# Optimization experiments

Hardware: AMD Instinct MI355X
Metric: run time of the kernel (lower is better)

Reference implementation:

```python
import jax, jax.numpy as jnp
import numpy as np

B = 16        # graphs per protein batch
NPG = 2000    # nodes per graph
N = B * NPG   # total nodes
E = 640000    # total edges
H, C = 3, 128 # heads, hidden_dim
FIN = 1038
K = 400       # ceil(0.2 * NPG) SAGPool keep count
NEG = 0.1     # LeakyReLU slope in model
EPS = 1e-5


def setup_inputs() -> dict:
    key = jax.random.key(0)
    ks = jax.random.split(key, 24)
    d = {}
    d['p1_x'] = jax.random.normal(ks[0], (N, FIN), jnp.float32)
    d['p2_x'] = jax.random.normal(ks[1], (N, FIN), jnp.float32)
    d['p1_edge_index'] = jax.random.randint(ks[2], (2, E), 0, N, jnp.int32)
    d['p2_edge_index'] = jax.random.randint(ks[3], (2, E), 0, N, jnp.int32)
    d['p1_edge_attr'] = jax.random.uniform(ks[4], (E, 2), jnp.float32)
    d['p2_edge_attr'] = jax.random.uniform(ks[5], (E, 2), jnp.float32)
    s_in = 1.0 / np.sqrt(FIN)
    s_h = 1.0 / np.sqrt(C)
    # GATv2Conv params (lin_l has bias, lin_r no bias, lin_edge, att, out bias)
    d['Wl'] = jax.random.normal(ks[6], (FIN, H * C), jnp.float32) * s_in
    d['bl'] = jnp.zeros((H * C,), jnp.float32)
    d['Wr'] = jax.random.normal(ks[7], (FIN, H * C), jnp.float32) * s_in
    d['We'] = jax.random.normal(ks[8], (2, H * C), jnp.float32) * 0.5
    d['att'] = jax.random.normal(ks[9], (H, C), jnp.float32) * s_h
    d['conv_bias'] = jnp.zeros((C,), jnp.float32)
    # BatchNorm1d
    d['gamma'] = jnp.ones((C,), jnp.float32)
    d['beta'] = jnp.zeros((C,), jnp.float32)
    # SAGPooling scorer: GraphConv(C -> 1)
    d['gc_Wrel'] = jax.random.normal(ks[10], (C, 1), jnp.float32) * s_h
    d['gc_Wroot'] = jax.random.normal(ks[11], (C, 1), jnp.float32) * s_h
    d['gc_b'] = jnp.zeros((1,), jnp.float32)
    # MLP head
    d['W1'] = jax.random.normal(ks[12], (2 * C, C), jnp.float32) / np.sqrt(2 * C)
    d['b1'] = jnp.zeros((C,), jnp.float32)
    d['W2'] = jax.random.normal(ks[13], (C, C // 2), jnp.float32) * s_h
    d['b2'] = jnp.zeros((C // 2,), jnp.float32)
    d['Wo'] = jax.random.normal(ks[14], (C // 2, 1), jnp.float32) / np.sqrt(C // 2)
    d['bo'] = jnp.zeros((1,), jnp.float32)
    return d


def gatv2(x, ei, ea, Wl, bl, Wr, We, att, conv_bias):
    # GATv2Conv, heads=3, concat=False, edge_dim=2, add_self_loops (fill='mean')
    loop = jnp.arange(N, dtype=ei.dtype)
    src = jnp.concatenate([ei[0], loop])
    dst = jnp.concatenate([ei[1], loop])
    ea_full = jnp.concatenate([ea, jnp.broadcast_to(ea.mean(0), (N, ea.shape[1]))], 0)
    xl = (x @ Wl + bl).reshape(N, H, C)
    xr = (x @ Wr).reshape(N, H, C)
    ef = (ea_full @ We).reshape(-1, H, C)
    m = xl[src] + xr[dst] + ef                      # [E+N, H, C]
    e = jnp.einsum('ehc,hc->eh', jax.nn.leaky_relu(m, 0.2), att)
    emax = jax.ops.segment_max(e, dst, num_segments=N)
    ex = jnp.exp(e - emax[dst])
    denom = jax.ops.segment_sum(ex, dst, num_segments=N)
    alpha = ex / denom[dst]                          # softmax per dst node, per head
    out = jax.ops.segment_sum(alpha[:, :, None] * xl[src], dst, num_segments=N)
    return out.mean(1) + conv_bias                   # concat=False -> head mean


def branch(x, ei, ea, Wl, bl, Wr, We, att, conv_bias, gamma, beta,
           gc_Wrel, gc_Wroot, gc_b):
    h = gatv2(x, ei, ea, Wl, bl, Wr, We, att, conv_bias)
    h = jax.nn.leaky_relu(h, NEG)
    mu = h.mean(0)
    var = ((h - mu) ** 2).mean(0)
    h = (h - mu) / jnp.sqrt(var + EPS) * gamma + beta  # BatchNorm1d (batch stats)
    # SAGPooling scorer: GraphConv out_i = W_root x_i + W_rel sum_{j->i} x_j + b
    agg = jax.ops.segment_sum(h[ei[0]], ei[1], num_segments=N)
    score = jnp.tanh((h @ gc_Wroot + agg @ gc_Wrel + gc_b)[:, 0])  # [N]
    s = score.reshape(B, NPG)
    topv, topi = jax.lax.top_k(s, K)                 # per-graph top-k
    hb = h.reshape(B, NPG, C)
    hsel = jnp.take_along_axis(hb, topi[:, :, None], axis=1)  # [B, K, C]
    hsel = hsel * topv[:, :, None]                   # x[perm] * tanh(score)[perm]
    return hsel.mean(1)                              # global mean pool -> [B, C]


def reference(p1_x, p2_x, p1_edge_attr, p2_edge_attr, Wl, bl, Wr, We, att,
              conv_bias, gamma, beta, gc_Wrel, gc_Wroot, gc_b, W1, b1, W2, b2,
              Wo, bo, p1_edge_index, p2_edge_index):
    x1 = branch(p1_x, p1_edge_index, p1_edge_attr, Wl, bl, Wr, We, att,
                conv_bias, gamma, beta, gc_Wrel, gc_Wroot, gc_b)
    x2 = branch(p2_x, p2_edge_index, p2_edge_attr, Wl, bl, Wr, We, att,
                conv_bias, gamma, beta, gc_Wrel, gc_Wroot, gc_b)
    xc = jnp.concatenate([x1, x2], 1)                # [B, 2C]
    xc = jax.nn.leaky_relu(xc @ W1 + b1, NEG)
    xc = jax.nn.leaky_relu(xc @ W2 + b2, NEG)
    return jax.nn.sigmoid(xc @ Wo + bo)              # [B, 1]
```

## Files before the change

kernel.cpp:

```cpp
#include <hip/hip_runtime.h>
#include <hip/hip_bf16.h>
#include <math.h>

#define NN 32000
#define EE 640000
#define CC 128
#define HC 384
#define FIN 1038
#define KP 1056
#define KT 33
#define BB 16
#define NPG 2000
#define KK 400

#define XLR_H  12288000u
#define HBN_STR 4096000u
#define OFF_STR 32064u

#define XH_OFF     0u
#define XL_OFF     16896000u
#define XR_OFF     29184000u
#define HBN_OFF    41472000u
#define SED_OFF    49664000u
#define CNT_OFF    52224000u
#define BNSUM_OFF  52288000u
#define BNSQ_OFF   52288256u
#define MEANEA_OFF 52288512u
#define ZERO_BYTES ((52288516u - 52224000u) * 4u)
#define OFFS_OFF   52288576u
#define CUR_OFF    52352704u
#define R_OFF      52416704u
#define REL_OFF    52480704u
#define SCORE_OFF  52544704u
#define XB_OFF     52608704u
#define WTH_OFF    52612800u

typedef __attribute__((ext_vector_type(8))) _Float16 f16x8;
typedef __attribute__((ext_vector_type(2))) _Float16 f16x2;
typedef __attribute__((ext_vector_type(4))) float f32x4;
typedef __attribute__((ext_vector_type(8))) unsigned short us8;

typedef const __attribute__((address_space(1))) unsigned int* gp1_t;
typedef __attribute__((address_space(3))) unsigned int* lp3_t;
__device__ __forceinline__ void gl_lds16(const void* g, void* l) {
    __builtin_amdgcn_global_load_lds((gp1_t)g, (lp3_t)l, 16, 0, 0);
}

__global__ __launch_bounds__(256) void k_prep(const int* __restrict__ ei0, const int* __restrict__ ei1,
                                              const float* __restrict__ ea0, const float* __restrict__ ea1,
                                              int* __restrict__ cnt, float* __restrict__ meanea) {
    int b = blockIdx.x;
    int br = (b >= 2500);
    int tid = threadIdx.x;
    int e = (b - br * 2500) * 256 + tid;
    const int* ei = br ? ei1 : ei0;
    const float* ea = br ? ea1 : ea0;
    cnt += br * NN; meanea += br * 2;
    float s0 = 0.f, s1 = 0.f;
    if (e < EE) {
        atomicAdd(&cnt[ei[EE + e]], 1);
        float2 t = ((const float2*)ea)[e];
        s0 = t.x; s1 = t.y;
    }
    __shared__ float r0[256], r1[256];
    r0[tid] = s0; r1[tid] = s1; __syncthreads();
    for (int st = 128; st; st >>= 1) {
        if (tid < st) { r0[tid] += r0[tid + st]; r1[tid] += r1[tid + st]; }
        __syncthreads();
    }
    if (tid == 0) { atomicAdd(&meanea[0], r0[0]); atomicAdd(&meanea[1], r1[0]); }
}

__global__ __launch_bounds__(1024) void k_scan(const int* __restrict__ cnt, int* __restrict__ offs, int* __restrict__ cur) {
    int br = blockIdx.x;
    cnt += br * NN; offs += br * OFF_STR; cur += br * NN;
    __shared__ int sb[1024];
    int tid = threadIdx.x;
    int base = tid * 32;
    int s = 0;
    for (int i = 0; i < 32; i++) { int idx = base + i; s += (idx < NN) ? cnt[idx] : 0; }
    sb[tid] = s; __syncthreads();
    for (int off = 1; off < 1024; off <<= 1) {
        int v = (tid >= off) ? sb[tid - off] : 0;
        __syncthreads();
        sb[tid] += v;
        __syncthreads();
    }
    int run = sb[tid] - s;
    for (int i = 0; i < 32; i++) {
        int idx = base + i;
        if (idx < NN) { int c = cnt[idx]; offs[idx] = run; cur[idx] = run; run += c; }
    }
    if (tid == 1023) offs[NN] = run;
}

__global__ __launch_bounds__(256) void k_scatter(const int* __restrict__ ei0, const int* __restrict__ ei1,
                                                 const float* __restrict__ ea0, const float* __restrict__ ea1,
                                                 int* __restrict__ cur, int2* __restrict__ sed) {
    int b = blockIdx.x;
    int br = (b >= 2500);
    int e = (b - br * 2500) * 256 + threadIdx.x;
    const int* ei = br ? ei1 : ei0;
    const float* ea = br ? ea1 : ea0;
    cur += br * NN; sed += br * EE;
    if (e < EE) {
        int d = ei[EE + e];
        int p = atomicAdd(&cur[d], 1);
        float2 t = ((const float2*)ea)[e];
        f16x2 h; h[0] = (_Float16)t.x; h[1] = (_Float16)t.y;
        int2 pk;
        pk.x = ei[e];
        pk.y = __builtin_bit_cast(int, h);
        sed[p] = pk;
    }
}

__global__ __launch_bounds__(256) void k_cvtW(const float* __restrict__ Wl_, const float* __restrict__ Wr_,
                                              unsigned short* __restrict__ Bh) {
    int idx = blockIdx.x * 256 + threadIdx.x;
    if (idx >= 768 * (KP / 8)) return;
    int n = idx / (KP / 8);
    int seg = idx - n * (KP / 8);
    int c0 = seg * 8;
    const float* W = (n < HC) ? Wl_ : Wr_;
    int nc = (n < HC) ? n : n - HC;
    us8 h8;
#pragma unroll
    for (int j = 0; j < 8; ++j) {
        int k = c0 + j;
        float v = (k < FIN) ? W[(size_t)k * HC + nc] : 0.f;
        _Float16 h = (_Float16)v;
        h8[j] = __builtin_bit_cast(unsigned short, h);
    }
    *(us8*)&Bh[(size_t)n * KP + c0] = h8;
}

__global__ __launch_bounds__(256) void k_cvtX(const float* __restrict__ x, _Float16* __restrict__ xh) {
    int idx = blockIdx.x * 256 + threadIdx.x;
    if (idx >= NN * (KP / 8)) return;
    int row = idx / (KP / 8);
    int c8 = idx - row * (KP / 8);
    int col = c8 * 8;
    const float* gp = x + (size_t)row * FIN + col;
    f16x8 o;
    if (col + 8 <= FIN) {
        float2 v01 = ((const float2*)gp)[0];
        float2 v23 = ((const float2*)gp)[1];
        float2 v45 = ((const float2*)gp)[2];
        float2 v67 = ((const float2*)gp)[3];
        o[0] = (_Float16)v01.x; o[1] = (_Float16)v01.y;
        o[2] = (_Float16)v23.x; o[3] = (_Float16)v23.y;
        o[4] = (_Float16)v45.x; o[5] = (_Float16)v45.y;
        o[6] = (_Float16)v67.x; o[7] = (_Float16)v67.y;
    } else {
#pragma unroll
        for (int j = 0; j < 8; ++j) o[j] = (_Float16)((col + j < FIN) ? gp[j] : 0.f);
    }
    *(f16x8*)&xh[(size_t)row * KP + col] = o;
}

__global__ __launch_bounds__(256) void k_gemm3(const _Float16* __restrict__ xh,
                                               const unsigned short* __restrict__ Bh,
                                               const float* __restrict__ bias, int br,
                                               float* __restrict__ ws) {
    __shared__ _Float16 sA[128 * 32], sB[128 * 32];
    const int b2 = blockIdx.x;
    const int xcd = b2 & 7, slot = b2 >> 3;
    const int t = xcd * 188 + slot;
    if (t >= 1500) return;
    const int mt = t / 6, nt = t - mt * 6;
    const int bm = mt * 128, bn = nt * 128;

    _Float16* xlh = (_Float16*)(ws + XL_OFF) + (size_t)br * XLR_H;
    _Float16* xrh = (_Float16*)(ws + XR_OFF) + (size_t)br * XLR_H;

    const int tid = threadIdx.x;
    const int wave = tid >> 6, lane = tid & 63;
    const int wm = (wave >> 1) * 64, wn = (wave & 1) * 64;
    const int quad = lane >> 4, l15 = lane & 15;

    const int srow = wave * 16 + (lane >> 2);
    const int scol = (lane & 3) * 8;
    const size_t gA0 = (size_t)(bm + srow) * KP + scol;
    const size_t gA1 = (size_t)(bm + 64 + srow) * KP + scol;
    const size_t gB0 = (size_t)(bn + srow) * KP + scol;
    const size_t gB1 = (size_t)(bn + 64 + srow) * KP + scol;
    const int lds0 = (wave * 16) * 32 + lane * 8;
    const int lds1 = (64 + wave * 16) * 32 + lane * 8;

    f32x4 acc[4][4];
#pragma unroll
    for (int i = 0; i < 4; ++i)
#pragma unroll
        for (int j = 0; j < 4; ++j) {
            f32x4 z = {0.f, 0.f, 0.f, 0.f};
            acc[i][j] = z;
        }

    const int aoff0 = (wm + l15) * 32 + quad * 8;
    const int boff0 = (wn + l15) * 32 + quad * 8;

    for (int kt = 0; kt < KT; ++kt) {
        const int kc = kt * 32;
        gl_lds16(xh + gA0 + kc, &sA[lds0]);
        gl_lds16(xh + gA1 + kc, &sA[lds1]);
        gl_lds16(Bh + gB0 + kc, &sB[lds0]);
        gl_lds16(Bh + gB1 + kc, &sB[lds1]);
        __syncthreads();
        f16x8 bfr[4];
#pragma unroll
        for (int j = 0; j < 4; ++j) bfr[j] = *(const f16x8*)&sB[boff0 + j * 512];
#pragma unroll
        for (int i = 0; i < 4; ++i) {
            f16x8 a = *(const f16x8*)&sA[aoff0 + i * 512];
#pragma unroll
            for (int j = 0; j < 4; ++j)
                acc[i][j] = __builtin_amdgcn_mfma_f32_16x16x32_f16(a, bfr[j], acc[i][j], 0, 0, 0);
        }
        __syncthreads();
    }

    const bool isL = (nt < 3);
    if (isL) {
#pragma unroll
        for (int j = 0; j < 4; ++j) {
            const int ncol = wn + j * 16 + l15;
            const float bj = bias[bn + ncol];
#pragma unroll
            for (int i = 0; i < 4; ++i) {
#pragma unroll
                for (int r = 0; r < 4; ++r) {
                    int m = bm + wm + i * 16 + quad * 4 + r;
                    xlh[(size_t)m * HC + bn + ncol] = (_Float16)(acc[i][j][r] + bj);
                }
            }
        }
    } else {
        const int nbase = bn - HC;
#pragma unroll
        for (int j = 0; j < 4; ++j) {
            const int ncol = wn + j * 16 + l15;
#pragma unroll
            for (int i = 0; i < 4; ++i) {
#pragma unroll
                for (int r = 0; r < 4; ++r) {
                    int m = bm + wm + i * 16 + quad * 4 + r;
                    xrh[(size_t)m * HC + nbase + ncol] = (_Float16)acc[i][j][r];
                }
            }
        }
    }
}

__global__ __launch_bounds__(256) void k_gat(const unsigned short* __restrict__ xlhb, const unsigned short* __restrict__ xrhb,
                                             const int* __restrict__ offsb, const int2* __restrict__ sedb,
                                             const float* __restrict__ meaneab,
                                             const float* __restrict__ We, const float* __restrict__ att,
                                             const float* __restrict__ conv_bias, float* __restrict__ houtb) {
    int gwave = (blockIdx.x * 256 + threadIdx.x) >> 6;
    int lane = threadIdx.x & 63;
    int half = lane >> 5, l32 = lane & 31;
    int br = (gwave >= NN);
    int node = gwave - br * NN;
    const _Float16* xlh = (const _Float16*)xlhb + (size_t)br * XLR_H;
    const _Float16* xrh = (const _Float16*)xrhb + (size_t)br * XLR_H;
    const int* offs = offsb + br * OFF_STR;
    const int2* sed = sedb + br * EE;
    const float* meanea = meaneab + br * 2;
    float* hout = houtb + br * HBN_STR;

    f16x2 we0p[6], we1p[6], attp[6], xrp[6];
    const f16x2* xrw = (const f16x2*)(xrh + (size_t)node * HC);
#pragma unroll
    for (int jj = 0; jj < 6; ++jj) {
        int q = l32 + 32 * jj;
        float2 w0 = ((const float2*)We)[q];
        float2 w1 = ((const float2*)(We + HC))[q];
        float2 av = ((const float2*)att)[q];
        we0p[jj][0] = (_Float16)w0.x; we0p[jj][1] = (_Float16)w0.y;
        we1p[jj][0] = (_Float16)w1.x; we1p[jj][1] = (_Float16)w1.y;
        attp[jj][0] = (_Float16)av.x; attp[jj][1] = (_Float16)av.y;
        xrp[jj] = xrw[q];
    }
    _Float16 meh0 = (_Float16)(meanea[0] * (1.0f / EE));
    _Float16 meh1 = (_Float16)(meanea[1] * (1.0f / EE));

    int p0 = offs[node], p1 = offs[node + 1];
    int cntE = p1 - p0;
    int iters = (cntE + 2) >> 1;

    float den0 = 0.f, den1 = 0.f, den2 = 0.f;
    float accv[12];
#pragma unroll
    for (int k = 0; k < 12; ++k) accv[k] = 0.f;

    const f16x2 zero2 = {(_Float16)0.f, (_Float16)0.f};
    const f16x2 c02 = {(_Float16)0.2f, (_Float16)0.2f};

    for (int i = 0; i < iters; ++i) {
        int t = 2 * i + half;
        bool self = (t == 0);
        bool valid = (t <= cntE);
        int p = p0 + t - 1;
        if (p < p0) p = p0;
        if (p > EE - 1) p = EE - 1;
        int2 pk = sed[p];
        f16x2 eh = __builtin_bit_cast(f16x2, pk.y);
        int s = self ? node : pk.x;
        _Float16 e0 = self ? meh0 : eh[0];
        _Float16 e1 = self ? meh1 : eh[1];
        f16x2 e0p, e1p;
        e0p[0] = e0; e0p[1] = e0;
        e1p[0] = e1; e1p[1] = e1;

        const f16x2* xrow = (const f16x2*)(xlh + (size_t)s * HC);
        f16x2 xv[6];
#pragma unroll
        for (int jj = 0; jj < 6; ++jj) xv[jj] = xrow[l32 + 32 * jj];

        float pr0 = 0.f, pr1 = 0.f, pr2 = 0.f;
#pragma unroll
        for (int jj = 0; jj < 6; ++jj) {
            f16x2 u = xrp[jj] + e0p * we0p[jj];
            u = u + e1p * we1p[jj];
            f16x2 m = xv[jj] + u;
            f16x2 mx = __builtin_elementwise_max(m, zero2);
            f16x2 mn = __builtin_elementwise_min(m, zero2);
            f16x2 lk = mx + mn * c02;
#if __has_builtin(__builtin_amdgcn_fdot2)
            if (jj < 2)      pr0 = __builtin_amdgcn_fdot2(lk, attp[jj], pr0, false);
            else if (jj < 4) pr1 = __builtin_amdgcn_fdot2(lk, attp[jj], pr1, false);
            else             pr2 = __builtin_amdgcn_fdot2(lk, attp[jj], pr2, false);
#else
            float c = (float)lk[0] * (float)attp[jj][0] + (float)lk[1] * (float)attp[jj][1];
            if (jj < 2) pr0 += c; else if (jj < 4) pr1 += c; else pr2 += c;
#endif
        }
#pragma unroll
        for (int msk = 16; msk; msk >>= 1) {
            pr0 += __shfl_xor(pr0, msk);
            pr1 += __shfl_xor(pr1, msk);
            pr2 += __shfl_xor(pr2, msk);
        }
        float w0 = valid ? __expf(pr0) : 0.f;
        float w1 = valid ? __expf(pr1) : 0.f;
        float w2 = valid ? __expf(pr2) : 0.f;
        den0 += w0; den1 += w1; den2 += w2;
#pragma unroll
        for (int jj = 0; jj < 6; ++jj) {
            float wh = (jj < 2) ? w0 : ((jj < 4) ? w1 : w2);
            accv[2 * jj]     += wh * (float)xv[jj][0];
            accv[2 * jj + 1] += wh * (float)xv[jj][1];
        }
    }

#pragma unroll
    for (int k = 0; k < 12; ++k) accv[k] += __shfl_xor(accv[k], 32);
    den0 += __shfl_xor(den0, 32);
    den1 += __shfl_xor(den1, 32);
    den2 += __shfl_xor(den2, 32);

    if (half == 0) {
        float i0 = 1.f / den0, i1 = 1.f / den1, i2 = 1.f / den2;
#pragma unroll
        for (int jja = 0; jja < 2; ++jja) {
#pragma unroll
            for (int b = 0; b < 2; ++b) {
                int c = (((jja * 32 + l32) << 1) | b);
                float o = (accv[2 * jja + b] * i0 + accv[2 * (jja + 2) + b] * i1 +
                           accv[2 * (jja + 4) + b] * i2) * (1.f / 3.f) + conv_bias[c];
                o = (o > 0.f) ? o : 0.1f * o;
                hout[(size_t)node * CC + c] = o;
            }
        }
    }
}

__global__ __launch_bounds__(256) void k_bnstats(const float* __restrict__ hb, float* __restrict__ bnsumb, float* __restrict__ bnsqb) {
    int b = blockIdx.x;
    int br = b >> 9, lb = b & 511;
    const float* h = hb + br * HBN_STR;
    float* bnsum = bnsumb + br * CC;
    float* bnsq = bnsqb + br * CC;
    int c = threadIdx.x & 127;
    int row0 = lb * 2 + (threadIdx.x >> 7);
    float s = 0.f, ss = 0.f;
    for (int n = row0; n < NN; n += 1024) {
        float v = h[(size_t)n * CC + c];
        s += v; ss += v * v;
    }
    atomicAdd(&bnsum[c], s);
    atomicAdd(&bnsq[c], ss);
}

__global__ __launch_bounds__(256) void k_bnapply(float* __restrict__ hb, const float* __restrict__ bnsumb,
                                                 const float* __restrict__ bnsqb,
                                                 const float* __restrict__ gamma, const float* __restrict__ beta,
                                                 const float* __restrict__ wroot,
                                                 const float* __restrict__ wrel, float* __restrict__ r_b, float* __restrict__ rel_b) {
    int gwave = (blockIdx.x * 256 + threadIdx.x) >> 6;
    int lane = threadIdx.x & 63;
    int br = (gwave >= NN);
    int wave = gwave - br * NN;
    float* h = hb + br * HBN_STR;
    const float* bnsum = bnsumb + br * CC;
    const float* bnsq = bnsqb + br * CC;
    float* r_ = r_b + br * NN;
    float* rel_ = rel_b + br * NN;

    float mu0 = bnsum[lane] * (1.f / NN);
    float var0 = bnsq[lane] * (1.f / NN) - mu0 * mu0;
    float sc0 = gamma[lane] * rsqrtf(var0 + 1e-5f);
    float sh0 = beta[lane] - mu0 * sc0;
    float mu1 = bnsum[64 + lane] * (1.f / NN);
    float var1 = bnsq[64 + lane] * (1.f / NN) - mu1 * mu1;
    float sc1 = gamma[64 + lane] * rsqrtf(var1 + 1e-5f);
    float sh1 = beta[64 + lane] - mu1 * sc1;

    size_t base = (size_t)wave * CC;
    float v0 = h[base + lane], v1 = h[base + 64 + lane];
    v0 = v0 * sc0 + sh0;
    v1 = v1 * sc1 + sh1;
    h[base + lane] = v0;
    h[base + 64 + lane] = v1;
    float pr = v0 * wroot[lane] + v1 * wroot[64 + lane];
    float pl = v0 * wrel[lane] + v1 * wrel[64 + lane];
#pragma unroll
    for (int m = 32; m; m >>= 1) {
        pr += __shfl_xor(pr, m);
        pl += __shfl_xor(pl, m);
    }
    if (lane == 0) { r_[wave] = pr; rel_[wave] = pl; }
}

__global__ __launch_bounds__(256) void k_score(const float* __restrict__ r_b, const float* __restrict__ rel_b,
                                               const int* __restrict__ offsb, const int2* __restrict__ sedb,
                                               const float* __restrict__ gcb, float* __restrict__ scoreb) {
    int gwave = (blockIdx.x * 256 + threadIdx.x) >> 6;
    int lane = threadIdx.x & 63;
    int br = (gwave >= NN);
    int wave = gwave - br * NN;
    const float* r_ = r_b + br * NN;
    const float* rel_ = rel_b + br * NN;
    const int* offs = offsb + br * OFF_STR;
    const int2* sed = sedb + br * EE;
    float* score = scoreb + br * NN;
    int p0 = offs[wave], p1 = offs[wave + 1];
    float s = 0.f;
    for (int p = p0 + lane; p < p1; p += 64) s += rel_[sed[p].x];
#pragma unroll
    for (int m = 32; m; m >>= 1) s += __shfl_xor(s, m);
    if (lane == 0) score[wave] = tanhf(r_[wave] + s + gcb[0]);
}

__global__ __launch_bounds__(1024) void k_topk(const float* __restrict__ scoreb, const float* __restrict__ hb,
                                               float* __restrict__ xbout) {
    __shared__ float sv[2048];
    __shared__ int si[2048];
    __shared__ float red[8][128];
    int b = blockIdx.x, tid = threadIdx.x;
    int br = b >> 4, g = b & 15;
    const float* score = scoreb + br * NN;
    const float* h = hb + br * HBN_STR;
    for (int i = tid; i < 2048; i += 1024) {
        sv[i] = (i < NPG) ? score[g * NPG + i] : -2.0f;
        si[i] = i;
    }
    __syncthreads();
    for (int k = 2; k <= 2048; k <<= 1) {
        for (int j = k >> 1; j > 0; j >>= 1) {
            for (int t = tid; t < 2048; t += 1024) {
                int ixj = t ^ j;
                if (ixj > t) {
                    bool up = ((t & k) == 0);
                    float a = sv[t], bv = sv[ixj];
                    bool sw = up ? (a < bv) : (a > bv);
                    if (sw) {
                        sv[t] = bv; sv[ixj] = a;
                        int tmp = si[t]; si[t] = si[ixj]; si[ixj] = tmp;
                    }
                }
            }
            __syncthreads();
        }
    }
    int grp = tid >> 7, c = tid & 127;
    float a = 0.f;
    for (int kk = grp; kk < KK; kk += 8) {
        int node = g * NPG + si[kk];
        a += sv[kk] * h[(size_t)node * CC + c];
    }
    red[grp][c] = a;
    __syncthreads();
    if (tid < 128) {
        float v = (red[0][tid] + red[1][tid] + red[2][tid] + red[3][tid] +
                   red[4][tid] + red[5][tid] + red[6][tid] + red[7][tid]) * (1.f / KK);
        xbout[(br * BB + g) * CC + tid] = v;
    }
}

__global__ __launch_bounds__(128) void k_mlp(const float* __restrict__ xb, const float* __restrict__ W1,
                                             const float* __restrict__ b1, const float* __restrict__ W2,
                                             const float* __restrict__ b2, const float* __restrict__ Wo,
                                             const float* __restrict__ bo, float* __restrict__ out) {
    int g = blockIdx.x, tid = threadIdx.x;
    __shared__ float xc[256], l1[128], l2[64];
    xc[tid] = xb[g * CC + tid];
    xc[128 + tid] = xb[BB * CC + g * CC + tid];
    __syncthreads();
    float s = b1[tid];
    for (int i = 0; i < 256; i++) s += xc[i] * W1[i * 128 + tid];
    l1[tid] = (s > 0.f) ? s : 0.1f * s;
    __syncthreads();
    if (tid < 64) {
        float s2 = b2[tid];
        for (int i = 0; i < 128; i++) s2 += l1[i] * W2[i * 64 + tid];
        l2[tid] = (s2 > 0.f) ? s2 : 0.1f * s2;
    }
    __syncthreads();
    if (tid < 64) {
        float p = l2[tid] * Wo[tid];
#pragma unroll
        for (int m = 32; m; m >>= 1) p += __shfl_xor(p, m);
        if (tid == 0) out[g] = 1.f / (1.f + __expf(-(p + bo[0])));
    }
}

extern "C" void kernel_launch(void* const* d_in, const int* in_sizes, int n_in,
                              void* d_out, int out_size, void* d_ws, size_t ws_size,
                              hipStream_t stream) {
    (void)in_sizes; (void)n_in; (void)out_size; (void)ws_size;
    const float* x0   = (const float*)d_in[0];
    const float* x1   = (const float*)d_in[1];
    const int*   ei0  = (const int*)d_in[2];
    const int*   ei1  = (const int*)d_in[3];
    const float* ea0  = (const float*)d_in[4];
    const float* ea1  = (const float*)d_in[5];
    const float* Wl   = (const float*)d_in[6];
    const float* bl   = (const float*)d_in[7];
    const float* Wr   = (const float*)d_in[8];
    const float* We   = (const float*)d_in[9];
    const float* att  = (const float*)d_in[10];
    const float* cb   = (const float*)d_in[11];
    const float* gam  = (const float*)d_in[12];
    const float* bet  = (const float*)d_in[13];
    const float* wrel = (const float*)d_in[14];
    const float* wroot= (const float*)d_in[15];
    const float* gcb  = (const float*)d_in[16];
    const float* W1   = (const float*)d_in[17];
    const float* b1   = (const float*)d_in[18];
    const float* W2   = (const float*)d_in[19];
    const float* b2   = (const float*)d_in[20];
    const float* Wo   = (const float*)d_in[21];
    const float* bo   = (const float*)d_in[22];

    float* ws = (float*)d_ws;
    _Float16* xh  = (_Float16*)(ws + XH_OFF);
    unsigned short* xlh = (unsigned short*)(ws + XL_OFF);
    unsigned short* xrh = (unsigned short*)(ws + XR_OFF);
    float*  hbn   = ws + HBN_OFF;
    int2*   sed   = (int2*)(ws + SED_OFF);
    int*    cnt   = (int*)(ws + CNT_OFF);
    float*  bnsum = ws + BNSUM_OFF;
    float*  bnsq  = ws + BNSQ_OFF;
    float*  meanea= ws + MEANEA_OFF;
    int*    offs  = (int*)(ws + OFFS_OFF);
    int*    cur   = (int*)(ws + CUR_OFF);
    float*  r_    = ws + R_OFF;
    float*  rel_  = ws + REL_OFF;
    float*  score = ws + SCORE_OFF;
    float*  xb    = ws + XB_OFF;
    unsigned short* Wth = (unsigned short*)(ws + WTH_OFF);

    hipMemsetAsync(cnt, 0, ZERO_BYTES, stream);
    k_cvtW<<<(768 * (KP / 8) + 255) / 256, 256, 0, stream>>>(Wl, Wr, Wth);

    k_prep<<<5000, 256, 0, stream>>>(ei0, ei1, ea0, ea1, cnt, meanea);
    k_scan<<<2, 1024, 0, stream>>>(cnt, offs, cur);
    k_scatter<<<5000, 256, 0, stream>>>(ei0, ei1, ea0, ea1, cur, sed);

    k_cvtX<<<(NN * (KP / 8) + 255) / 256, 256, 0, stream>>>(x0, xh);
    k_gemm3<<<1504, 256, 0, stream>>>(xh, Wth, bl, 0, ws);
    k_cvtX<<<(NN * (KP / 8) + 255) / 256, 256, 0, stream>>>(x1, xh);
    k_gemm3<<<1504, 256, 0, stream>>>(xh, Wth, bl, 1, ws);

    k_gat<<<16000, 256, 0, stream>>>(xlh, xrh, offs, sed, meanea, We, att, cb, hbn);

    k_bnstats<<<1024, 256, 0, stream>>>(hbn, bnsum, bnsq);
    k_bnapply<<<16000, 256, 0, stream>>>(hbn, bnsum, bnsq, gam, bet, wroot, wrel, r_, rel_);
    k_score<<<16000, 256, 0, stream>>>(r_, rel_, offs, sed, gcb, score);
    k_topk<<<32, 1024, 0, stream>>>(score, hbn, xb);

    k_mlp<<<BB, 128, 0, stream>>>(xb, W1, b1, W2, b2, Wo, bo, (float*)d_out);
}
```

Before: 1.153 ms.

## Double-buffer GEMM LDS tiles, permute xl/xr layout, halve score wave width

The GEMM now double-buffers its LDS tiles and issues the next K-slice's global-to-LDS loads before computing the current one, which halves the barriers per iteration and overlaps load latency with MFMA work. The GEMM epilogue writes xl/xr columns in a permuted order so each GAT lane reads 12 contiguous halves as three 8-byte vector loads instead of six strided 4-byte loads. The score kernel uses 32 lanes per node instead of 64, halving the grid and cutting idle lanes for low-degree nodes. The costs are double the LDS footprint in the GEMM and more scattered stores in the GEMM epilogue.

```diff
diff --git a/kernel.cpp b/kernel.cpp
--- a/kernel.cpp
+++ b/kernel.cpp
@@ -36,6 +36,7 @@
 #define WTH_OFF    52612800u
 
 typedef __attribute__((ext_vector_type(8))) _Float16 f16x8;
+typedef __attribute__((ext_vector_type(4))) _Float16 f16x4;
 typedef __attribute__((ext_vector_type(2))) _Float16 f16x2;
 typedef __attribute__((ext_vector_type(4))) float f32x4;
 typedef __attribute__((ext_vector_type(8))) unsigned short us8;
@@ -44,6 +45,11 @@
 typedef __attribute__((address_space(3))) unsigned int* lp3_t;
 __device__ __forceinline__ void gl_lds16(const void* g, void* l) {
     __builtin_amdgcn_global_load_lds((gp1_t)g, (lp3_t)l, 16, 0, 0);
+}
+
+__device__ __forceinline__ int permoff(int c) {
+    int q = c >> 1, b = c & 1;
+    return ((((q & 31) * 6) + (q >> 5)) << 1) | b;
 }
 
 __global__ __launch_bounds__(256) void k_prep(const int* __restrict__ ei0, const int* __restrict__ ei1,
@@ -163,7 +169,7 @@
                                                const unsigned short* __restrict__ Bh,
                                                const float* __restrict__ bias, int br,
                                                float* __restrict__ ws) {
-    __shared__ _Float16 sA[128 * 32], sB[128 * 32];
+    __shared__ _Float16 sA[2][128 * 32], sB[2][128 * 32];
     const int b2 = blockIdx.x;
     const int xcd = b2 & 7, slot = b2 >> 3;
     const int t = xcd * 188 + slot;
@@ -200,25 +206,33 @@
     const int aoff0 = (wm + l15) * 32 + quad * 8;
     const int boff0 = (wn + l15) * 32 + quad * 8;
 
+#define STAGE(KT_, BUF_) do {                          \
+        const int kc_ = (KT_) * 32;                    \
+        gl_lds16(xh + gA0 + kc_, &sA[BUF_][lds0]);     \
+        gl_lds16(xh + gA1 + kc_, &sA[BUF_][lds1]);     \
+        gl_lds16(Bh + gB0 + kc_, &sB[BUF_][lds0]);     \
+        gl_lds16(Bh + gB1 + kc_, &sB[BUF_][lds1]);     \
+    } while (0)
+
+    STAGE(0, 0);
+    __syncthreads();
+
     for (int kt = 0; kt < KT; ++kt) {
-        const int kc = kt * 32;
-        gl_lds16(xh + gA0 + kc, &sA[lds0]);
-        gl_lds16(xh + gA1 + kc, &sA[lds1]);
-        gl_lds16(Bh + gB0 + kc, &sB[lds0]);
-        gl_lds16(Bh + gB1 + kc, &sB[lds1]);
-        __syncthreads();
+        const int cur = kt & 1, nxt = cur ^ 1;
+        if (kt + 1 < KT) STAGE(kt + 1, nxt);
         f16x8 bfr[4];
 #pragma unroll
-        for (int j = 0; j < 4; ++j) bfr[j] = *(const f16x8*)&sB[boff0 + j * 512];
+        for (int j = 0; j < 4; ++j) bfr[j] = *(const f16x8*)&sB[cur][boff0 + j * 512];
 #pragma unroll
         for (int i = 0; i < 4; ++i) {
-            f16x8 a = *(const f16x8*)&sA[aoff0 + i * 512];
+            f16x8 a = *(const f16x8*)&sA[cur][aoff0 + i * 512];
 #pragma unroll
             for (int j = 0; j < 4; ++j)
                 acc[i][j] = __builtin_amdgcn_mfma_f32_16x16x32_f16(a, bfr[j], acc[i][j], 0, 0, 0);
         }
         __syncthreads();
     }
+#undef STAGE
 
     const bool isL = (nt < 3);
     if (isL) {
@@ -226,12 +240,13 @@
         for (int j = 0; j < 4; ++j) {
             const int ncol = wn + j * 16 + l15;
             const float bj = bias[bn + ncol];
+            const int off = permoff(bn + ncol);
 #pragma unroll
             for (int i = 0; i < 4; ++i) {
 #pragma unroll
                 for (int r = 0; r < 4; ++r) {
                     int m = bm + wm + i * 16 + quad * 4 + r;
-                    xlh[(size_t)m * HC + bn + ncol] = (_Float16)(acc[i][j][r] + bj);
+                    xlh[(size_t)m * HC + off] = (_Float16)(acc[i][j][r] + bj);
                 }
             }
         }
@@ -240,12 +255,13 @@
 #pragma unroll
         for (int j = 0; j < 4; ++j) {
             const int ncol = wn + j * 16 + l15;
+            const int off = permoff(nbase + ncol);
 #pragma unroll
             for (int i = 0; i < 4; ++i) {
 #pragma unroll
                 for (int r = 0; r < 4; ++r) {
                     int m = bm + wm + i * 16 + quad * 4 + r;
-                    xrh[(size_t)m * HC + nbase + ncol] = (_Float16)acc[i][j][r];
+                    xrh[(size_t)m * HC + off] = (_Float16)acc[i][j][r];
                 }
             }
         }
@@ -270,7 +286,6 @@
     float* hout = houtb + br * HBN_STR;
 
     f16x2 we0p[6], we1p[6], attp[6], xrp[6];
-    const f16x2* xrw = (const f16x2*)(xrh + (size_t)node * HC);
 #pragma unroll
     for (int jj = 0; jj < 6; ++jj) {
         int q = l32 + 32 * jj;
@@ -280,7 +295,15 @@
         we0p[jj][0] = (_Float16)w0.x; we0p[jj][1] = (_Float16)w0.y;
         we1p[jj][0] = (_Float16)w1.x; we1p[jj][1] = (_Float16)w1.y;
         attp[jj][0] = (_Float16)av.x; attp[jj][1] = (_Float16)av.y;
-        xrp[jj] = xrw[q];
+    }
+    {
+        const _Float16* xrrow = xrh + (size_t)node * HC + l32 * 12;
+        f16x4 r0 = *(const f16x4*)(xrrow);
+        f16x4 r1 = *(const f16x4*)(xrrow + 4);
+        f16x4 r2 = *(const f16x4*)(xrrow + 8);
+        xrp[0][0] = r0[0]; xrp[0][1] = r0[1]; xrp[1][0] = r0[2]; xrp[1][1] = r0[3];
+        xrp[2][0] = r1[0]; xrp[2][1] = r1[1]; xrp[3][0] = r1[2]; xrp[3][1] = r1[3];
+        xrp[4][0] = r2[0]; xrp[4][1] = r2[1]; xrp[5][0] = r2[2]; xrp[5][1] = r2[3];
     }
     _Float16 meh0 = (_Float16)(meanea[0] * (1.0f / EE));
     _Float16 meh1 = (_Float16)(meanea[1] * (1.0f / EE));
@@ -313,10 +336,14 @@
         e0p[0] = e0; e0p[1] = e0;
         e1p[0] = e1; e1p[1] = e1;
 
-        const f16x2* xrow = (const f16x2*)(xlh + (size_t)s * HC);
+        const _Float16* xrow = xlh + (size_t)s * HC + l32 * 12;
+        f16x4 v0 = *(const f16x4*)(xrow);
+        f16x4 v1 = *(const f16x4*)(xrow + 4);
+        f16x4 v2 = *(const f16x4*)(xrow + 8);
         f16x2 xv[6];
-#pragma unroll
-        for (int jj = 0; jj < 6; ++jj) xv[jj] = xrow[l32 + 32 * jj];
+        xv[0][0] = v0[0]; xv[0][1] = v0[1]; xv[1][0] = v0[2]; xv[1][1] = v0[3];
+        xv[2][0] = v1[0]; xv[2][1] = v1[1]; xv[3][0] = v1[2]; xv[3][1] = v1[3];
+        xv[4][0] = v2[0]; xv[4][1] = v2[1]; xv[5][0] = v2[2]; xv[5][1] = v2[3];
 
         float pr0 = 0.f, pr1 = 0.f, pr2 = 0.f;
 #pragma unroll
@@ -436,21 +463,21 @@
 __global__ __launch_bounds__(256) void k_score(const float* __restrict__ r_b, const float* __restrict__ rel_b,
                                                const int* __restrict__ offsb, const int2* __restrict__ sedb,
                                                const float* __restrict__ gcb, float* __restrict__ scoreb) {
-    int gwave = (blockIdx.x * 256 + threadIdx.x) >> 6;
-    int lane = threadIdx.x & 63;
-    int br = (gwave >= NN);
-    int wave = gwave - br * NN;
+    int gw = (blockIdx.x * 256 + threadIdx.x) >> 5;
+    int l32 = threadIdx.x & 31;
+    int br = (gw >= NN);
+    int node = gw - br * NN;
     const float* r_ = r_b + br * NN;
     const float* rel_ = rel_b + br * NN;
     const int* offs = offsb + br * OFF_STR;
     const int2* sed = sedb + br * EE;
     float* score = scoreb + br * NN;
-    int p0 = offs[wave], p1 = offs[wave + 1];
+    int p0 = offs[node], p1 = offs[node + 1];
     float s = 0.f;
-    for (int p = p0 + lane; p < p1; p += 64) s += rel_[sed[p].x];
-#pragma unroll
-    for (int m = 32; m; m >>= 1) s += __shfl_xor(s, m);
-    if (lane == 0) score[wave] = tanhf(r_[wave] + s + gcb[0]);
+    for (int p = p0 + l32; p < p1; p += 32) s += rel_[sed[p].x];
+#pragma unroll
+    for (int m = 16; m; m >>= 1) s += __shfl_xor(s, m);
+    if (l32 == 0) score[node] = tanhf(r_[node] + s + gcb[0]);
 }
 
 __global__ __launch_bounds__(1024) void k_topk(const float* __restrict__ scoreb, const float* __restrict__ hb,
@@ -588,7 +615,7 @@
 
     k_bnstats<<<1024, 256, 0, stream>>>(hbn, bnsum, bnsq);
     k_bnapply<<<16000, 256, 0, stream>>>(hbn, bnsum, bnsq, gam, bet, wroot, wrel, r_, rel_);
-    k_score<<<16000, 256, 0, stream>>>(r_, rel_, offs, sed, gcb, score);
+    k_score<<<8000, 256, 0, stream>>>(r_, rel_, offs, sed, gcb, score);
     k_topk<<<32, 1024, 0, stream>>>(score, hbn, xb);
 
     k_mlp<<<BB, 128, 0, stream>>>(xb, W1, b1, W2, b2, Wo, bo, (float*)d_out);
```

Measured after the change: 1.214 ms. 5.3% more time.
